# Kernel tuning notes

Hardware: AMD Instinct MI355X
Metric: run time of the kernel (lower is better)

## Reference

```python
import jax, jax.numpy as jnp
import numpy as np

N_NODES = 384
IN_F = 128
HID = 256
NUM_RBF = 50
NUM_BASIS = 8
NUM_HEADS = 8
HEAD_D = HID // NUM_HEADS
INT_OUT = 2 * NUM_RBF * NUM_BASIS            # K and Q, each num_rbf*num_basis
NODE_OUT = NUM_BASIS * NUM_BASIS + 2 * NUM_BASIS  # W0, B0, W1


def setup_inputs() -> dict:
    key = jax.random.key(0)
    ks = jax.random.split(key, 13)
    s = 0.05
    def p(k, shape):
        return jax.random.normal(k, shape, jnp.float32) * s
    return {
        "h": jax.random.normal(ks[0], (N_NODES, IN_F), jnp.float32),
        "fc_w": p(ks[1], (HID, IN_F)),
        "fc_b": p(ks[2], (HID,)),
        "in_proj_w": p(ks[3], (3 * HID, HID)),
        "in_proj_b": p(ks[4], (3 * HID,)),
        "out_proj_w": p(ks[5], (HID, HID)),
        "out_proj_b": p(ks[6], (HID,)),
        "fci_w1": p(ks[7], (HID, 2 * HID)),
        "fci_b1": p(ks[8], (HID,)),
        "fci_w2": p(ks[9], (INT_OUT, HID)),
        "fci_b2": p(ks[10], (INT_OUT,)),
        "fcn_w": p(ks[11], (NODE_OUT, HID)),
        "fcn_b": p(ks[12], (NODE_OUT,)),
    }


def reference(h, fc_w, fc_b, in_proj_w, in_proj_b, out_proj_w, out_proj_b,
              fci_w1, fci_b1, fci_w2, fci_b2, fcn_w, fcn_b):
    n = h.shape[0]
    # input projection
    h = h @ fc_w.T + fc_b                                   # (n, HID)
    # multihead self-attention (torch nn.MultiheadAttention math)
    qkv = h @ in_proj_w.T + in_proj_b                       # (n, 3*HID)
    q, k, v = jnp.split(qkv, 3, axis=-1)
    def heads(x):
        return x.reshape(n, NUM_HEADS, HEAD_D).transpose(1, 0, 2)  # (H, n, D)
    q, k, v = heads(q), heads(k), heads(v)
    scores = jnp.einsum('hnd,hmd->hnm', q, k) / jnp.sqrt(jnp.asarray(HEAD_D, h.dtype))
    attn = jax.nn.softmax(scores, axis=-1)
    h = jnp.einsum('hnm,hmd->hnd', attn, v).transpose(1, 0, 2).reshape(n, HID)
    h = h @ out_proj_w.T + out_proj_b                       # (n, HID)
    # pairwise interaction: h_interaction[i, j] = concat(h[j], h[i])
    # first Linear split algebraically: cat(hj, hi) @ W1.T = hj@Wa.T + hi@Wb.T
    wa, wb = fci_w1[:, :HID], fci_w1[:, HID:]
    pre = (h @ wa.T)[None, :, :] + (h @ wb.T)[:, None, :] + fci_b1  # (n, n, HID)
    kq = jnp.tanh(pre) @ fci_w2.T + fci_b2                  # (n, n, INT_OUT)
    K, Q = jnp.split(kq, 2, axis=-1)
    K = K.reshape(n, n, NUM_RBF, NUM_BASIS)
    Q = Q.reshape(n, n, NUM_RBF, NUM_BASIS)
    # node-wise parameters
    node = h @ fcn_w.T + fcn_b                              # (n, NODE_OUT)
    b2 = NUM_BASIS * NUM_BASIS
    W0 = node[:, :b2].reshape(n, NUM_BASIS, NUM_BASIS)
    B0 = node[:, b2:b2 + NUM_BASIS]
    W1 = node[:, b2 + NUM_BASIS:].reshape(n, NUM_BASIS, 1)
    return (K, Q, W0, B0, W1)
```

## Files before the change

kernel.cpp:

```cpp
#include <hip/hip_runtime.h>
#include <hip/hip_bf16.h>

typedef __attribute__((ext_vector_type(8))) short bf16x8;
typedef __attribute__((ext_vector_type(4))) float f32x4;

static __device__ __forceinline__ unsigned int f2bf(float f) {
    unsigned int u = __float_as_uint(f);
    u = u + 0x7FFFu + ((u >> 16) & 1u);
    return (u >> 16);
}

static __device__ __forceinline__ float fast_tanh(float x) {
    x = fminf(fmaxf(x, -10.f), 10.f);
    float e = __expf(2.f * x);
    return __fdividef(e - 1.f, e + 1.f);
}

#define LGKM_BAR() do {                                      \
    asm volatile("s_waitcnt lgkmcnt(0)" ::: "memory");       \
    __builtin_amdgcn_s_barrier();                            \
} while (0)

__global__ __launch_bounds__(256)
void prep(const float* __restrict__ fc_w, const float* __restrict__ inp_w,
          const float* __restrict__ outp_w, const float* __restrict__ fci_w1,
          const float* __restrict__ fcn_w, const float* __restrict__ fci_w2,
          float* __restrict__ fcwT, float* __restrict__ inpT,
          float* __restrict__ outpT, float* __restrict__ waT,
          float* __restrict__ wbT, float* __restrict__ fcnT,
          uint4* __restrict__ w2p)
{
    const int idx0 = blockIdx.x * 256 + threadIdx.x;
    const int stride = 64 * 256;
    switch (blockIdx.y) {
    case 0:
        for (int c = idx0; c < 32768; c += stride) {
            int k = c >> 8, n = c & 255;
            fcwT[c] = fc_w[n * 128 + k];
        }
        break;
    case 1:
        for (int c = idx0; c < 196608; c += stride) {
            int k = c / 768, n = c - k * 768;
            inpT[c] = inp_w[n * 256 + k];
        }
        break;
    case 2:
        for (int c = idx0; c < 65536; c += stride) {
            int k = c >> 8, n = c & 255;
            outpT[c] = outp_w[n * 256 + k];
        }
        break;
    case 3:
        for (int c = idx0; c < 65536; c += stride) {
            int k = c >> 8, n = c & 255;
            waT[c] = fci_w1[n * 512 + k];
        }
        break;
    case 4:
        for (int c = idx0; c < 65536; c += stride) {
            int k = c >> 8, n = c & 255;
            wbT[c] = fci_w1[n * 512 + 256 + k];
        }
        break;
    case 5:
        for (int c = idx0; c < 20480; c += stride) {
            int k = c / 80, n = c - k * 80;
            fcnT[c] = fcn_w[n * 256 + k];
        }
        break;
    default:
        for (int c = idx0; c < 25600; c += stride) {
            const int n_g = c >> 5, e = c & 31;
            const int kk = e >> 2, kg = e & 3;
            const int ph = (n_g >= 400) ? 1 : 0;
            const int n = n_g - ph * 400;
            const float4* s = (const float4*)(fci_w2 + n_g * 256 + kk * 32 + kg * 8);
            const float4 x0 = s[0], x1 = s[1];
            uint4 pk;
            pk.x = f2bf(x0.x) | (f2bf(x0.y) << 16);
            pk.y = f2bf(x0.z) | (f2bf(x0.w) << 16);
            pk.z = f2bf(x1.x) | (f2bf(x1.y) << 16);
            pk.w = f2bf(x1.z) | (f2bf(x1.w) << 16);
            w2p[((ph * 8 + kk) * 400 + n) * 4 + kg] = pk;
        }
        break;
    }
}

__global__ __launch_bounds__(256)
void k1_rows(const float* __restrict__ h, const float* __restrict__ fc_b,
             const float* __restrict__ inp_b, const float* __restrict__ fcwT,
             const float* __restrict__ inpT, float* __restrict__ qkv)
{
    __shared__ float hrow[128];
    __shared__ float h1row[256];
    const int i = blockIdx.x, tid = threadIdx.x;
    if (tid < 128) hrow[tid] = h[i * 128 + tid];
    __syncthreads();
    float acc = fc_b[tid];
    #pragma unroll 8
    for (int k = 0; k < 128; ++k) acc += hrow[k] * fcwT[k * 256 + tid];
    h1row[tid] = acc;
    __syncthreads();
    float a0 = inp_b[tid], a1 = inp_b[tid + 256], a2 = inp_b[tid + 512];
    #pragma unroll 8
    for (int k = 0; k < 256; ++k) {
        const float f = h1row[k];
        a0 += f * inpT[k * 768 + tid];
        a1 += f * inpT[k * 768 + tid + 256];
        a2 += f * inpT[k * 768 + tid + 512];
    }
    qkv[i * 768 + tid] = a0;
    qkv[i * 768 + tid + 256] = a1;
    qkv[i * 768 + tid + 512] = a2;
}

__global__ __launch_bounds__(256)
void attn_kernel(const float* __restrict__ qkv, float* __restrict__ out)
{
    const int n = blockIdx.x;
    const int h = blockIdx.y;
    const int tid = threadIdx.x;
    const int lane = tid & 63;
    const int wid = tid >> 6;

    __shared__ float qs[32];
    __shared__ float p[384];
    __shared__ float red[8];
    __shared__ float pv[8][32];

    if (tid < 32) qs[tid] = qkv[n * 768 + h * 32 + tid] * 0.17677669529663687f;
    __syncthreads();

    float lmax = -1e30f;
    for (int m = tid; m < 384; m += 256) {
        const float4* kr = (const float4*)(qkv + m * 768 + 256 + h * 32);
        float s = 0.f;
        #pragma unroll
        for (int d = 0; d < 8; ++d) {
            float4 kv = kr[d];
            s += qs[d*4+0]*kv.x + qs[d*4+1]*kv.y + qs[d*4+2]*kv.z + qs[d*4+3]*kv.w;
        }
        p[m] = s;
        lmax = fmaxf(lmax, s);
    }
    #pragma unroll
    for (int off = 32; off >= 1; off >>= 1) lmax = fmaxf(lmax, __shfl_xor(lmax, off));
    if (lane == 0) red[wid] = lmax;
    __syncthreads();
    const float gmax = fmaxf(fmaxf(red[0], red[1]), fmaxf(red[2], red[3]));

    float lsum = 0.f;
    for (int m = tid; m < 384; m += 256) {
        float e = __expf(p[m] - gmax);
        p[m] = e;
        lsum += e;
    }
    #pragma unroll
    for (int off = 32; off >= 1; off >>= 1) lsum += __shfl_xor(lsum, off);
    if (lane == 0) red[4 + wid] = lsum;
    __syncthreads();
    const float inv = 1.f / (red[4] + red[5] + red[6] + red[7]);

    const int d = tid & 31;
    const int g = tid >> 5;
    float acc = 0.f;
    for (int m = g * 48; m < g * 48 + 48; ++m)
        acc += p[m] * qkv[m * 768 + 512 + h * 32 + d];
    pv[g][d] = acc;
    __syncthreads();
    if (tid < 32) {
        float o = 0.f;
        #pragma unroll
        for (int gg = 0; gg < 8; ++gg) o += pv[gg][tid];
        out[n * 256 + h * 32 + tid] = o * inv;
    }
}

__global__ __launch_bounds__(256)
void k3_rows(const float* __restrict__ attnO, const float* __restrict__ outp_b,
             const float* __restrict__ fci_b1, const float* __restrict__ fcn_b,
             const float* __restrict__ outpT, const float* __restrict__ waT,
             const float* __restrict__ wbT, const float* __restrict__ fcnT,
             float* __restrict__ hA, float* __restrict__ hB, float* __restrict__ out)
{
    __shared__ float arow[256];
    __shared__ float h2row[256];
    const int i = blockIdx.x, tid = threadIdx.x;
    arow[tid] = attnO[i * 256 + tid];
    __syncthreads();
    float acc = outp_b[tid];
    #pragma unroll 8
    for (int k = 0; k < 256; ++k) acc += arow[k] * outpT[k * 256 + tid];
    h2row[tid] = acc;
    __syncthreads();
    float aA = fci_b1[tid], aB = 0.f;
    #pragma unroll 8
    for (int k = 0; k < 256; ++k) {
        const float f = h2row[k];
        aA += f * waT[k * 256 + tid];
        aB += f * wbT[k * 256 + tid];
    }
    hA[i * 256 + tid] = aA;
    hB[i * 256 + tid] = aB;
    if (tid < 80) {
        float aN = fcn_b[tid];
        #pragma unroll 8
        for (int k = 0; k < 256; ++k) aN += h2row[k] * fcnT[k * 80 + tid];
        if (tid < 64)      out[117964800 + i * 64 + tid] = aN;
        else if (tid < 72) out[117989376 + i * 8 + (tid - 64)] = aN;
        else               out[117992448 + i * 8 + (tid - 72)] = aN;
    }
}

#define CSM_ROW 1616

__global__ __launch_bounds__(320)
void gen_kq(const float* __restrict__ hA, const float* __restrict__ hB,
            const uint4* __restrict__ w2p, const float* __restrict__ b2,
            float* __restrict__ outK, float* __restrict__ outQ)
{
    __shared__ unsigned char Aim[48 * 512];
    __shared__ unsigned char Csm[16 * CSM_ROW];

    const int tid  = threadIdx.x;
    const int lane = tid & 63;
    const int wn   = tid >> 6;
    const int lr   = lane & 15;
    const int kg   = lane >> 4;

    const int bid = blockIdx.x;
    const int m0  = bid * 48;
    const int ai  = bid >> 3;
    const int bj0 = (bid & 7) * 48;

    for (int c = tid; c < 1536; c += 320) {
        const int row = c >> 5;
        const int e   = c & 31;
        const int ke  = e * 8;
        const float4 a0 = *(const float4*)(hA + (bj0 + row) * 256 + ke);
        const float4 a1 = *(const float4*)(hA + (bj0 + row) * 256 + ke + 4);
        const float4 b0 = *(const float4*)(hB + ai * 256 + ke);
        const float4 b1 = *(const float4*)(hB + ai * 256 + ke + 4);
        uint4 pk;
        pk.x = f2bf(fast_tanh(a0.x + b0.x)) | (f2bf(fast_tanh(a0.y + b0.y)) << 16);
        pk.y = f2bf(fast_tanh(a0.z + b0.z)) | (f2bf(fast_tanh(a0.w + b0.w)) << 16);
        pk.z = f2bf(fast_tanh(a1.x + b1.x)) | (f2bf(fast_tanh(a1.y + b1.y)) << 16);
        pk.w = f2bf(fast_tanh(a1.z + b1.z)) | (f2bf(fast_tanh(a1.w + b1.w)) << 16);
        *(uint4*)(Aim + row * 512 + ((e * 16) ^ ((row & 7) << 4))) = pk;
    }
    LGKM_BAR();

    #pragma unroll
    for (int ph = 0; ph < 2; ++ph) {
        f32x4 acc[3][5];
        #pragma unroll
        for (int j = 0; j < 5; ++j) {
            const float4 bb = *(const float4*)(b2 + ph * 400 + wn * 80 + j * 16 + kg * 4);
            #pragma unroll
            for (int i = 0; i < 3; ++i)
                acc[i][j] = (f32x4){bb.x, bb.y, bb.z, bb.w};
        }

        #pragma unroll 2
        for (int kk = 0; kk < 8; ++kk) {
            bf16x8 af_[3], bf_[5];
            const uint4* wb = w2p + (ph * 8 + kk) * 1600;
            #pragma unroll
            for (int j = 0; j < 5; ++j)
                bf_[j] = *(const bf16x8*)(wb + (wn * 80 + j * 16 + lr) * 4 + kg);
            #pragma unroll
            for (int i = 0; i < 3; ++i) {
                const int row = i * 16 + lr;
                af_[i] = *(const bf16x8*)(Aim + row * 512 +
                          ((kk * 64 + kg * 16) ^ ((row & 7) << 4)));
            }
            #pragma unroll
            for (int i = 0; i < 3; ++i)
                #pragma unroll
                for (int j = 0; j < 5; ++j)
                    acc[i][j] = __builtin_amdgcn_mfma_f32_16x16x32_bf16(
                        bf_[j], af_[i], acc[i][j], 0, 0, 0);
        }

        float* gob = ph ? outQ : outK;
        #pragma unroll
        for (int p = 0; p < 3; ++p) {
            {
                const int i = p;
                #pragma unroll
                for (int j = 0; j < 5; ++j) {
                    float4 v;
                    v.x = acc[i][j][0]; v.y = acc[i][j][1];
                    v.z = acc[i][j][2]; v.w = acc[i][j][3];
                    *(float4*)(Csm + lr * CSM_ROW + (wn * 80 + j * 16 + kg * 4) * 4) = v;
                }
            }
            LGKM_BAR();
            {
                float* gb = gob + (size_t)m0 * 400 + p * 6400;
                #pragma unroll
                for (int q = 0; q < 5; ++q) {
                    const int f = q * 320 + tid;
                    const int row = f / 100, c4 = f - row * 100;
                    const float4 v = *(const float4*)(Csm + row * CSM_ROW + c4 * 16);
                    *(float4*)(gb + f * 4) = v;
                }
            }
            LGKM_BAR();
        }
    }
}

extern "C" void kernel_launch(void* const* d_in, const int* in_sizes, int n_in,
                              void* d_out, int out_size, void* d_ws, size_t ws_size,
                              hipStream_t stream)
{
    (void)in_sizes; (void)n_in; (void)out_size; (void)ws_size;

    const float* h      = (const float*)d_in[0];
    const float* fc_w   = (const float*)d_in[1];
    const float* fc_b   = (const float*)d_in[2];
    const float* inp_w  = (const float*)d_in[3];
    const float* inp_b  = (const float*)d_in[4];
    const float* outp_w = (const float*)d_in[5];
    const float* outp_b = (const float*)d_in[6];
    const float* fci_w1 = (const float*)d_in[7];
    const float* fci_b1 = (const float*)d_in[8];
    const float* fci_w2 = (const float*)d_in[9];
    const float* fci_b2 = (const float*)d_in[10];
    const float* fcn_w  = (const float*)d_in[11];
    const float* fcn_b  = (const float*)d_in[12];

    float* out  = (float*)d_out;
    float* outK = out;
    float* outQ = out + 58982400;

    float* ws    = (float*)d_ws;
    float* qkv   = ws;
    float* attnO = qkv   + 294912;
    float* hA    = attnO + 98304;
    float* hBv   = hA    + 98304;
    float* fcwT  = hBv   + 98304;
    float* inpT  = fcwT  + 32768;
    float* outpT = inpT  + 196608;
    float* waT   = outpT + 65536;
    float* wbT   = waT   + 65536;
    float* fcnT  = wbT   + 65536;
    uint4* w2p   = (uint4*)(fcnT + 20480);

    prep<<<dim3(64, 7), 256, 0, stream>>>(fc_w, inp_w, outp_w, fci_w1, fcn_w, fci_w2,
                                          fcwT, inpT, outpT, waT, wbT, fcnT, w2p);
    k1_rows<<<384, 256, 0, stream>>>(h, fc_b, inp_b, fcwT, inpT, qkv);
    attn_kernel<<<dim3(384, 8), 256, 0, stream>>>(qkv, attnO);
    k3_rows<<<384, 256, 0, stream>>>(attnO, outp_b, fci_b1, fcn_b, outpT, waT, wbT, fcnT,
                                     hA, hBv, out);
    gen_kq<<<dim3(3072), 320, 0, stream>>>(hA, hBv, w2p, fci_b2, outK, outQ);
}
```

Measured before the change: 234.6 us.

## Store MFMA results directly to global with nontemporal stores, drop LDS staging

Replaces the shared-memory staging of the output tile (write accumulators to LDS, barrier, coalesced reread and store) with direct per-lane 16-byte nontemporal global stores from the MFMA accumulators. It also alternates which half (K or Q) each block computes first, so neighbouring blocks write to different output regions. The aim is to remove LDS traffic and barriers and to stop the large write-only output from polluting the cache. The tradeoff is less coalesced writes, since each lane writes 16 bytes at a 1600-byte row stride rather than contiguous rows.

```diff
diff --git a/kernel.cpp b/kernel.cpp
--- a/kernel.cpp
+++ b/kernel.cpp
@@ -214,15 +214,12 @@
     }
 }
 
-#define CSM_ROW 1616
-
 __global__ __launch_bounds__(320)
 void gen_kq(const float* __restrict__ hA, const float* __restrict__ hB,
             const uint4* __restrict__ w2p, const float* __restrict__ b2,
             float* __restrict__ outK, float* __restrict__ outQ)
 {
     __shared__ unsigned char Aim[48 * 512];
-    __shared__ unsigned char Csm[16 * CSM_ROW];
 
     const int tid  = threadIdx.x;
     const int lane = tid & 63;
@@ -252,15 +249,18 @@
     }
     LGKM_BAR();
 
+    const int phfirst = bid & 1;
     #pragma unroll
-    for (int ph = 0; ph < 2; ++ph) {
+    for (int pp = 0; pp < 2; ++pp) {
+        const int ph = pp ^ phfirst;
+
         f32x4 acc[3][5];
         #pragma unroll
         for (int j = 0; j < 5; ++j) {
-            const float4 bb = *(const float4*)(b2 + ph * 400 + wn * 80 + j * 16 + kg * 4);
+            const f32x4 bb = *(const f32x4*)(b2 + ph * 400 + wn * 80 + j * 16 + kg * 4);
             #pragma unroll
             for (int i = 0; i < 3; ++i)
-                acc[i][j] = (f32x4){bb.x, bb.y, bb.z, bb.w};
+                acc[i][j] = bb;
         }
 
         #pragma unroll 2
@@ -286,29 +286,11 @@
 
         float* gob = ph ? outQ : outK;
         #pragma unroll
-        for (int p = 0; p < 3; ++p) {
-            {
-                const int i = p;
-                #pragma unroll
-                for (int j = 0; j < 5; ++j) {
-                    float4 v;
-                    v.x = acc[i][j][0]; v.y = acc[i][j][1];
-                    v.z = acc[i][j][2]; v.w = acc[i][j][3];
-                    *(float4*)(Csm + lr * CSM_ROW + (wn * 80 + j * 16 + kg * 4) * 4) = v;
-                }
-            }
-            LGKM_BAR();
-            {
-                float* gb = gob + (size_t)m0 * 400 + p * 6400;
-                #pragma unroll
-                for (int q = 0; q < 5; ++q) {
-                    const int f = q * 320 + tid;
-                    const int row = f / 100, c4 = f - row * 100;
-                    const float4 v = *(const float4*)(Csm + row * CSM_ROW + c4 * 16);
-                    *(float4*)(gb + f * 4) = v;
-                }
-            }
-            LGKM_BAR();
+        for (int i = 0; i < 3; ++i) {
+            float* rbase = gob + (size_t)(m0 + i * 16 + lr) * 400 + wn * 80 + kg * 4;
+            #pragma unroll
+            for (int j = 0; j < 5; ++j)
+                __builtin_nontemporal_store(acc[i][j], (f32x4*)(rbase + j * 16));
         }
     }
 }
```

Measured after the change: 239.9 us. 2.2% more time.
